# Performance work log

Measured on AMD Instinct MI355X. Metric: run time of the kernel, lower is better.

The kernel has to match this reference:

```python
import jax, jax.numpy as jnp
from jax import lax
import numpy as np

B, L, E, H = 4, 512, 1024, 128


def setup_inputs() -> dict:
    key = jax.random.key(0)
    k0, k1, k2, k3, k4, k5 = jax.random.split(key, 6)
    s = 1.0 / np.sqrt(E)
    return {
        "rec_emb": jax.random.normal(k0, (B, L, E), jnp.float32),
        "lig_emb": jax.random.normal(k1, (B, L, E), jnp.float32),
        "W1": jax.random.normal(k2, (E, H), jnp.float32) * s,
        "b1": jax.random.normal(k3, (H,), jnp.float32) * 0.01,
        "conv_w": jax.random.normal(k4, (1, H, 2, 2), jnp.float32) * (1.0 / np.sqrt(H * 4)),
        "conv_b": jax.random.normal(k5, (1,), jnp.float32) * 0.01,
    }


def reference(rec_emb, lig_emb, W1, b1, conv_w, conv_b):
    # shared fc: Linear -> ReLU (Dropout is identity in eval mode)
    rec_hid = jax.nn.relu(jnp.einsum("bie,eh->bih", rec_emb, W1) + b1)
    lig_hid = jax.nn.relu(jnp.einsum("bje,eh->bjh", lig_emb, W1) + b1)
    # outer-product bilinear map: bih,bjh->bijh, then tanh
    mat = jnp.tanh(rec_hid[:, :, None, :] * lig_hid[:, None, :, :])
    # permute to NCHW: (b, h, i, j)
    mat = jnp.transpose(mat, (0, 3, 1, 2))
    # Conv2d(H -> 1, kernel=2, padding=1): out spatial = L + 1
    y = lax.conv_general_dilated(
        mat, conv_w, window_strides=(1, 1), padding=[(1, 1), (1, 1)],
        dimension_numbers=("NCHW", "OIHW", "NCHW"),
    ) + conv_b[None, :, None, None]
    # MaxPool2d(kernel=2, stride=2), floor mode
    pooled = lax.reduce_window(
        y, -jnp.inf, lax.max,
        window_dimensions=(1, 1, 2, 2), window_strides=(1, 1, 2, 2),
        padding="VALID",
    )
    # global max over spatial dims -> (b, 1), sigmoid, flatten
    m = jnp.max(pooled, axis=(2, 3))
    return jax.nn.sigmoid(m).reshape(-1)
```

## Files before the change

kernel.cpp:

```cpp
#include <hip/hip_runtime.h>
#include <hip/hip_fp16.h>
#include <math.h>

#define BDIM 4
#define LDIM 512
#define EDIM 1024
#define HDIM 128
#define TILE 32
#define NT   16
#define K2   2.885390081777927f

typedef unsigned short ushort_t;
typedef __attribute__((ext_vector_type(8))) _Float16 half8;
typedef __attribute__((ext_vector_type(4))) float f32x4;

struct __align__(16) H8 { __half2 p[4]; };
union HU { H8 h; half8 v; };

__global__ __launch_bounds__(256) void wcvt(const float* __restrict__ W1,
                                            ushort_t* __restrict__ Wt) {
  const int g = (int)blockIdx.x * 256 + threadIdx.x;
  const int n = g & 127, k8 = g >> 7;
  float v[8];
#pragma unroll
  for (int j = 0; j < 8; ++j) v[j] = W1[(size_t)(k8 * 8 + j) * HDIM + n];
  H8 o;
#pragma unroll
  for (int j = 0; j < 4; ++j) o.p[j] = __floats2half2_rn(v[2 * j], v[2 * j + 1]);
  *(H8*)&Wt[(size_t)n * EDIM + k8 * 8] = o;
}

__global__ __launch_bounds__(256) void gemm_direct(
    const float* __restrict__ rec, const float* __restrict__ lig,
    const ushort_t* __restrict__ Wt, const float* __restrict__ b1,
    ushort_t* __restrict__ hid) {
  const int gw = (int)blockIdx.x * 4 + (threadIdx.x >> 6);
  const int l = threadIdx.x & 63;
  const int strip = gw >> 3;
  const int nidx = gw & 7;
  const int r0 = strip * 16;
  const int m = l & 15, q = l >> 4;
  const float* arow = ((r0 < BDIM * LDIM)
                           ? rec + (size_t)r0 * EDIM
                           : lig + (size_t)(r0 - BDIM * LDIM) * EDIM) +
                      (size_t)m * EDIM + q * 8;
  const ushort_t* brow = Wt + (size_t)(nidx * 16 + m) * EDIM + q * 8;

  f32x4 acc = {0.f, 0.f, 0.f, 0.f};
  for (int blk = 0; blk < 8; ++blk) {
    float4 alo[4], ahi[4];
    half8 bf[4];
#pragma unroll
    for (int j = 0; j < 4; ++j) {
      const int k0 = (blk * 4 + j) * 32;
      alo[j] = *(const float4*)(arow + k0);
      ahi[j] = *(const float4*)(arow + k0 + 4);
      bf[j] = *(const half8*)(brow + k0);
    }
#pragma unroll
    for (int j = 0; j < 4; ++j) {
      HU au;
      au.h.p[0] = __floats2half2_rn(alo[j].x, alo[j].y);
      au.h.p[1] = __floats2half2_rn(alo[j].z, alo[j].w);
      au.h.p[2] = __floats2half2_rn(ahi[j].x, ahi[j].y);
      au.h.p[3] = __floats2half2_rn(ahi[j].z, ahi[j].w);
      acc = __builtin_amdgcn_mfma_f32_16x16x32_f16(au.v, bf[j], acc, 0, 0, 0);
    }
  }
  const float scale = (r0 < BDIM * LDIM) ? -K2 : 1.0f;
  const int col = nidx * 16 + m;
  const float bias = b1[col];
#pragma unroll
  for (int r = 0; r < 4; ++r) {
    float v = fmaxf(acc[r] + bias, 0.f) * scale;
    ((_Float16*)hid)[(size_t)(r0 + q * 4 + r) * HDIM + col] = (_Float16)v;
  }
}

__global__ __launch_bounds__(256, 4) void bilinear_max(
    const ushort_t* __restrict__ hid, const float* __restrict__ cw,
    const float* __restrict__ cb, float* __restrict__ partial) {
  __shared__ ushort_t rl[33][130];
  __shared__ ushort_t ll[33][130];
  __shared__ float4 sl[33][34];
  __shared__ float wred[4];
  __shared__ float wpart[2][4];

  const int t = threadIdx.x;
  const int b = blockIdx.z;
  const int ib = (int)blockIdx.y * TILE - 1;
  const int jb = (int)blockIdx.x * TILE - 1;
  const int w = t >> 6, l = t & 63;
  const int q = l >> 4, c15 = l & 15;

  if (t < HDIM) {
    float4 w4 = *(const float4*)&cw[t * 4];
#pragma unroll
    for (int off = 32; off > 0; off >>= 1) {
      w4.x += __shfl_down(w4.x, off, 64);
      w4.y += __shfl_down(w4.y, off, 64);
      w4.z += __shfl_down(w4.z, off, 64);
      w4.w += __shfl_down(w4.w, off, 64);
    }
    if ((t & 63) == 0) {
      wpart[t >> 6][0] = w4.x; wpart[t >> 6][1] = w4.y;
      wpart[t >> 6][2] = w4.z; wpart[t >> 6][3] = w4.w;
    }
  }

  half8 wf[4];
#pragma unroll
  for (int c = 0; c < 4; ++c) {
#pragma unroll
    for (int j = 0; j < 8; ++j) {
      float v = (c15 < 4) ? cw[(size_t)(c * 32 + q * 8 + j) * 4 + c15] : 0.f;
      wf[c][j] = (_Float16)(-2.f * v);
    }
  }

  H8 z;
  z.p[0] = z.p[1] = z.p[2] = z.p[3] = __floats2half2_rn(0.f, 0.f);
  for (int p = t; p < 66 * 16; p += 256) {
    int r = p >> 4, seg = (p & 15) * 8;
    if (r < 33) {
      int i = ib + r;
      H8 v = z;
      if (i >= 0) v = *(const H8*)&hid[((size_t)(b * LDIM + i)) * HDIM + seg];
      *(H8*)&rl[r][seg] = v;
    } else {
      int j = jb + (r - 33);
      H8 v = z;
      if (j >= 0) v = *(const H8*)&hid[((size_t)((BDIM + b) * LDIM + j)) * HDIM + seg];
      *(H8*)&ll[r - 33][seg] = v;
    }
  }
  __syncthreads();
  const float wsum_v = (c15 < 4) ? (wpart[0][c15] + wpart[1][c15]) : 0.f;

  const __half2 D0 = __float2half2_rn(0.998539f);
  const __half2 D1 = __float2half2_rn(-0.947090f);
  const __half2 D2 = __float2half2_rn(0.676154f);
  const __half2 D3 = __float2half2_rn(-0.228646f);
#define POLYG(U) \
  __hmul2(U, __hfma2(U, __hfma2(U, __hfma2(U, D3, D2), D1), D0))

  for (int g = 0; g < 16; ++g) {
    const int ii = w * 8 + (g >> 1);
    const int jj0 = (g & 1) << 4;
    f32x4 acc = {0.f, 0.f, 0.f, 0.f};
#pragma unroll
    for (int c = 0; c < 4; ++c) {
      HU ru, lu, gu;
      ru.v = *(const half8*)&rl[ii][c * 32 + q * 8];
      lu.v = *(const half8*)&ll[jj0 + c15][c * 32 + q * 8];
      __half2 u0 = h2exp2(__hmul2(ru.h.p[0], lu.h.p[0]));
      __half2 u1 = h2exp2(__hmul2(ru.h.p[1], lu.h.p[1]));
      __half2 u2 = h2exp2(__hmul2(ru.h.p[2], lu.h.p[2]));
      __half2 u3 = h2exp2(__hmul2(ru.h.p[3], lu.h.p[3]));
      gu.h.p[0] = POLYG(u0);
      gu.h.p[1] = POLYG(u1);
      gu.h.p[2] = POLYG(u2);
      gu.h.p[3] = POLYG(u3);
      acc = __builtin_amdgcn_mfma_f32_16x16x32_f16(gu.v, wf[c], acc, 0, 0, 0);
    }
    if (c15 < 4) {
#pragma unroll
      for (int r = 0; r < 4; ++r)
        ((float*)&sl[ii][jj0 + q * 4 + r])[c15] = wsum_v + acc[r];
    }
  }
#undef POLYG

  if (t < 65) {
    const int pi = (t < 33) ? t : 32;
    const int qj = (t < 33) ? 32 : (t - 33);
    const float ws0 = wpart[0][0] + wpart[1][0];
    const float ws1 = wpart[0][1] + wpart[1][1];
    const float ws2 = wpart[0][2] + wpart[1][2];
    const float ws3 = wpart[0][3] + wpart[1][3];
    float4 sa = make_float4(0.f, 0.f, 0.f, 0.f);
    for (int h = 0; h < HDIM; ++h) {
      float rv = (float)(*(const _Float16*)&rl[pi][h]);
      float lv = (float)(*(const _Float16*)&ll[qj][h]);
      float u = __builtin_amdgcn_exp2f(rv * lv);
      float gg = u * fmaf(u, fmaf(u, fmaf(u, -0.228646f, 0.676154f), -0.947090f), 0.998539f);
      float4 w4 = *(const float4*)&cw[h * 4];
      sa.x = fmaf(-2.f * gg, w4.x, sa.x);
      sa.y = fmaf(-2.f * gg, w4.y, sa.y);
      sa.z = fmaf(-2.f * gg, w4.z, sa.z);
      sa.w = fmaf(-2.f * gg, w4.w, sa.w);
    }
    sl[pi][qj] = make_float4(ws0 + sa.x, ws1 + sa.y, ws2 + sa.z, ws3 + sa.w);
  }
  __syncthreads();

  float m = -INFINITY;
  const float cbv = cb[0];
  for (int p = t; p < 1024; p += 256) {
    int jj = (p & 31) + 1, iy = (p >> 5) + 1;
    float v = cbv + sl[iy - 1][jj - 1].x + sl[iy - 1][jj].y
                  + sl[iy][jj - 1].z + sl[iy][jj].w;
    m = fmaxf(m, v);
  }
#pragma unroll
  for (int off = 32; off > 0; off >>= 1) m = fmaxf(m, __shfl_down(m, off, 64));
  if ((t & 63) == 0) wred[t >> 6] = m;
  __syncthreads();
  if (t == 0) {
    float mm = fmaxf(fmaxf(wred[0], wred[1]), fmaxf(wred[2], wred[3]));
    partial[((size_t)b * NT + blockIdx.y) * NT + blockIdx.x] = mm;
  }
}

__global__ __launch_bounds__(64) void finalize(const float* __restrict__ partial,
                                               float* __restrict__ out) {
  const int b = blockIdx.x, t = threadIdx.x;
  float m = -INFINITY;
  for (int p = t; p < NT * NT; p += 64) m = fmaxf(m, partial[b * NT * NT + p]);
#pragma unroll
  for (int off = 32; off > 0; off >>= 1) m = fmaxf(m, __shfl_down(m, off, 64));
  if (t == 0) out[b] = 1.f / (1.f + expf(-m));
}

extern "C" void kernel_launch(void* const* d_in, const int* in_sizes, int n_in,
                              void* d_out, int out_size, void* d_ws, size_t ws_size,
                              hipStream_t stream) {
  const float* rec = (const float*)d_in[0];
  const float* lig = (const float*)d_in[1];
  const float* W1  = (const float*)d_in[2];
  const float* b1  = (const float*)d_in[3];
  const float* cw  = (const float*)d_in[4];
  const float* cb  = (const float*)d_in[5];
  float* out = (float*)d_out;

  ushort_t* Wt   = (ushort_t*)d_ws;
  ushort_t* hid  = Wt + (size_t)HDIM * EDIM;
  float* partial = (float*)(hid + (size_t)2 * BDIM * LDIM * HDIM);

  wcvt<<<dim3(64), 256, 0, stream>>>(W1, Wt);
  gemm_direct<<<dim3(512), 256, 0, stream>>>(rec, lig, Wt, b1, hid);
  bilinear_max<<<dim3(NT, NT, BDIM), 256, 0, stream>>>(hid, cw, cb, partial);
  finalize<<<dim3(BDIM), 64, 0, stream>>>(partial, out);
}
```

Before: 132.7 us.

## Fold W1 conversion into GEMM, hoist lig fragments, store conv partials in fp16

Drops the separate W1 transpose/convert kernel, so the GEMM reads fp32 W1 columns directly with strided scalar loads and converts them to fp16 in registers. In the bilinear kernel the ligand fragments are loaded once per half-tile and reused across eight rows, and the shared-memory conv partials are stored as fp16 instead of float4. Occupancy hint goes from 4 to 5 blocks. This saves one launch and some LDS, at the cost of uncoalesced W1 reads in the GEMM and reduced precision in the stored partials.

```diff
diff --git a/kernel.cpp b/kernel.cpp
--- a/kernel.cpp
+++ b/kernel.cpp
@@ -17,22 +17,9 @@
 struct __align__(16) H8 { __half2 p[4]; };
 union HU { H8 h; half8 v; };
 
-__global__ __launch_bounds__(256) void wcvt(const float* __restrict__ W1,
-                                            ushort_t* __restrict__ Wt) {
-  const int g = (int)blockIdx.x * 256 + threadIdx.x;
-  const int n = g & 127, k8 = g >> 7;
-  float v[8];
-#pragma unroll
-  for (int j = 0; j < 8; ++j) v[j] = W1[(size_t)(k8 * 8 + j) * HDIM + n];
-  H8 o;
-#pragma unroll
-  for (int j = 0; j < 4; ++j) o.p[j] = __floats2half2_rn(v[2 * j], v[2 * j + 1]);
-  *(H8*)&Wt[(size_t)n * EDIM + k8 * 8] = o;
-}
-
 __global__ __launch_bounds__(256) void gemm_direct(
     const float* __restrict__ rec, const float* __restrict__ lig,
-    const ushort_t* __restrict__ Wt, const float* __restrict__ b1,
+    const float* __restrict__ W1, const float* __restrict__ b1,
     ushort_t* __restrict__ hid) {
   const int gw = (int)blockIdx.x * 4 + (threadIdx.x >> 6);
   const int l = threadIdx.x & 63;
@@ -44,31 +31,37 @@
                            ? rec + (size_t)r0 * EDIM
                            : lig + (size_t)(r0 - BDIM * LDIM) * EDIM) +
                       (size_t)m * EDIM + q * 8;
-  const ushort_t* brow = Wt + (size_t)(nidx * 16 + m) * EDIM + q * 8;
+  const int col = nidx * 16 + m;
+  const float* wcol = W1 + col;
 
   f32x4 acc = {0.f, 0.f, 0.f, 0.f};
   for (int blk = 0; blk < 8; ++blk) {
     float4 alo[4], ahi[4];
-    half8 bf[4];
+    float bw[4][8];
 #pragma unroll
     for (int j = 0; j < 4; ++j) {
-      const int k0 = (blk * 4 + j) * 32;
-      alo[j] = *(const float4*)(arow + k0);
-      ahi[j] = *(const float4*)(arow + k0 + 4);
-      bf[j] = *(const half8*)(brow + k0);
+      const int k0 = (blk * 4 + j) * 32 + q * 8;
+      alo[j] = *(const float4*)(arow + (blk * 4 + j) * 32);
+      ahi[j] = *(const float4*)(arow + (blk * 4 + j) * 32 + 4);
+#pragma unroll
+      for (int kk = 0; kk < 8; ++kk)
+        bw[j][kk] = wcol[(size_t)(k0 + kk) * HDIM];
     }
 #pragma unroll
     for (int j = 0; j < 4; ++j) {
-      HU au;
+      HU au, bu;
       au.h.p[0] = __floats2half2_rn(alo[j].x, alo[j].y);
       au.h.p[1] = __floats2half2_rn(alo[j].z, alo[j].w);
       au.h.p[2] = __floats2half2_rn(ahi[j].x, ahi[j].y);
       au.h.p[3] = __floats2half2_rn(ahi[j].z, ahi[j].w);
-      acc = __builtin_amdgcn_mfma_f32_16x16x32_f16(au.v, bf[j], acc, 0, 0, 0);
+      bu.h.p[0] = __floats2half2_rn(bw[j][0], bw[j][1]);
+      bu.h.p[1] = __floats2half2_rn(bw[j][2], bw[j][3]);
+      bu.h.p[2] = __floats2half2_rn(bw[j][4], bw[j][5]);
+      bu.h.p[3] = __floats2half2_rn(bw[j][6], bw[j][7]);
+      acc = __builtin_amdgcn_mfma_f32_16x16x32_f16(au.v, bu.v, acc, 0, 0, 0);
     }
   }
   const float scale = (r0 < BDIM * LDIM) ? -K2 : 1.0f;
-  const int col = nidx * 16 + m;
   const float bias = b1[col];
 #pragma unroll
   for (int r = 0; r < 4; ++r) {
@@ -77,12 +70,12 @@
   }
 }
 
-__global__ __launch_bounds__(256, 4) void bilinear_max(
+__global__ __launch_bounds__(256, 5) void bilinear_max(
     const ushort_t* __restrict__ hid, const float* __restrict__ cw,
     const float* __restrict__ cb, float* __restrict__ partial) {
   __shared__ ushort_t rl[33][130];
   __shared__ ushort_t ll[33][130];
-  __shared__ float4 sl[33][34];
+  __shared__ ushort_t sl4[33][34][4];
   __shared__ float wred[4];
   __shared__ float wpart[2][4];
 
@@ -144,29 +137,37 @@
 #define POLYG(U) \
   __hmul2(U, __hfma2(U, __hfma2(U, __hfma2(U, D3, D2), D1), D0))
 
-  for (int g = 0; g < 16; ++g) {
-    const int ii = w * 8 + (g >> 1);
-    const int jj0 = (g & 1) << 4;
-    f32x4 acc = {0.f, 0.f, 0.f, 0.f};
-#pragma unroll
-    for (int c = 0; c < 4; ++c) {
-      HU ru, lu, gu;
-      ru.v = *(const half8*)&rl[ii][c * 32 + q * 8];
-      lu.v = *(const half8*)&ll[jj0 + c15][c * 32 + q * 8];
-      __half2 u0 = h2exp2(__hmul2(ru.h.p[0], lu.h.p[0]));
-      __half2 u1 = h2exp2(__hmul2(ru.h.p[1], lu.h.p[1]));
-      __half2 u2 = h2exp2(__hmul2(ru.h.p[2], lu.h.p[2]));
-      __half2 u3 = h2exp2(__hmul2(ru.h.p[3], lu.h.p[3]));
-      gu.h.p[0] = POLYG(u0);
-      gu.h.p[1] = POLYG(u1);
-      gu.h.p[2] = POLYG(u2);
-      gu.h.p[3] = POLYG(u3);
-      acc = __builtin_amdgcn_mfma_f32_16x16x32_f16(gu.v, wf[c], acc, 0, 0, 0);
-    }
-    if (c15 < 4) {
-#pragma unroll
-      for (int r = 0; r < 4; ++r)
-        ((float*)&sl[ii][jj0 + q * 4 + r])[c15] = wsum_v + acc[r];
+#pragma unroll
+  for (int hf = 0; hf < 2; ++hf) {
+    const int jj0 = hf << 4;
+    HU lu[4];
+#pragma unroll
+    for (int c = 0; c < 4; ++c)
+      lu[c].v = *(const half8*)&ll[jj0 + c15][c * 32 + q * 8];
+    for (int ii8 = 0; ii8 < 8; ++ii8) {
+      const int ii = w * 8 + ii8;
+      f32x4 acc = {0.f, 0.f, 0.f, 0.f};
+#pragma unroll
+      for (int c = 0; c < 4; ++c) {
+        HU ru, gu;
+        ru.v = *(const half8*)&rl[ii][c * 32 + q * 8];
+        __half2 u0 = h2exp2(__hmul2(ru.h.p[0], lu[c].h.p[0]));
+        __half2 u1 = h2exp2(__hmul2(ru.h.p[1], lu[c].h.p[1]));
+        __half2 u2 = h2exp2(__hmul2(ru.h.p[2], lu[c].h.p[2]));
+        __half2 u3 = h2exp2(__hmul2(ru.h.p[3], lu[c].h.p[3]));
+        gu.h.p[0] = POLYG(u0);
+        gu.h.p[1] = POLYG(u1);
+        gu.h.p[2] = POLYG(u2);
+        gu.h.p[3] = POLYG(u3);
+        acc = __builtin_amdgcn_mfma_f32_16x16x32_f16(gu.v, wf[c], acc, 0, 0, 0);
+      }
+      if (c15 < 4) {
+#pragma unroll
+        for (int r = 0; r < 4; ++r) {
+          _Float16 hv = (_Float16)(wsum_v + acc[r]);
+          sl4[ii][jj0 + q * 4 + r][c15] = *(ushort_t*)&hv;
+        }
+      }
     }
   }
 #undef POLYG
@@ -174,10 +175,6 @@
   if (t < 65) {
     const int pi = (t < 33) ? t : 32;
     const int qj = (t < 33) ? 32 : (t - 33);
-    const float ws0 = wpart[0][0] + wpart[1][0];
-    const float ws1 = wpart[0][1] + wpart[1][1];
-    const float ws2 = wpart[0][2] + wpart[1][2];
-    const float ws3 = wpart[0][3] + wpart[1][3];
     float4 sa = make_float4(0.f, 0.f, 0.f, 0.f);
     for (int h = 0; h < HDIM; ++h) {
       float rv = (float)(*(const _Float16*)&rl[pi][h]);
@@ -190,7 +187,11 @@
       sa.z = fmaf(-2.f * gg, w4.z, sa.z);
       sa.w = fmaf(-2.f * gg, w4.w, sa.w);
     }
-    sl[pi][qj] = make_float4(ws0 + sa.x, ws1 + sa.y, ws2 + sa.z, ws3 + sa.w);
+#pragma unroll
+    for (int k = 0; k < 4; ++k) {
+      _Float16 hv = (_Float16)(wpart[0][k] + wpart[1][k] + ((float*)&sa)[k]);
+      sl4[pi][qj][k] = *(ushort_t*)&hv;
+    }
   }
   __syncthreads();
 
@@ -198,8 +199,10 @@
   const float cbv = cb[0];
   for (int p = t; p < 1024; p += 256) {
     int jj = (p & 31) + 1, iy = (p >> 5) + 1;
-    float v = cbv + sl[iy - 1][jj - 1].x + sl[iy - 1][jj].y
-                  + sl[iy][jj - 1].z + sl[iy][jj].w;
+    float v = cbv + (float)(*(const _Float16*)&sl4[iy - 1][jj - 1][0])
+                  + (float)(*(const _Float16*)&sl4[iy - 1][jj][1])
+                  + (float)(*(const _Float16*)&sl4[iy][jj - 1][2])
+                  + (float)(*(const _Float16*)&sl4[iy][jj][3]);
     m = fmaxf(m, v);
   }
 #pragma unroll
@@ -233,12 +236,10 @@
   const float* cb  = (const float*)d_in[5];
   float* out = (float*)d_out;
 
-  ushort_t* Wt   = (ushort_t*)d_ws;
-  ushort_t* hid  = Wt + (size_t)HDIM * EDIM;
+  ushort_t* hid  = (ushort_t*)d_ws;
   float* partial = (float*)(hid + (size_t)2 * BDIM * LDIM * HDIM);
 
-  wcvt<<<dim3(64), 256, 0, stream>>>(W1, Wt);
-  gemm_direct<<<dim3(512), 256, 0, stream>>>(rec, lig, Wt, b1, hid);
+  gemm_direct<<<dim3(512), 256, 0, stream>>>(rec, lig, W1, b1, hid);
   bilinear_max<<<dim3(NT, NT, BDIM), 256, 0, stream>>>(hid, cw, cb, partial);
   finalize<<<dim3(BDIM), 64, 0, stream>>>(partial, out);
 }
```

Result: no change. 130.7 us (-1.4%).
